# Kernel optimization log

Hardware: AMD Instinct MI355X
Metric: run time of the kernel (lower is better)

Reference implementation:

```python
import jax, jax.numpy as jnp
import numpy as np

N_NODES = 100000
N_EDGES = 1600000
NFEAT = 256
NHID = 128


def _l2_normalize(v, eps=1e-12):
    return v / (jnp.linalg.norm(v) + eps)


def setup_inputs() -> dict:
    key = jax.random.key(0)
    k1, k2, k3, k4 = jax.random.split(key, 4)
    x = jax.random.normal(k1, (N_NODES, NFEAT), dtype=jnp.float32)
    edge_index = jax.random.randint(k2, (2, N_EDGES), 0, N_NODES, dtype=jnp.int64)
    # GCNConv weight (glorot-ish scale), spectral-normalized at forward time
    W = jax.random.normal(k3, (NFEAT, NHID), dtype=jnp.float32) * 0.05
    bias = jnp.zeros((NHID,), dtype=jnp.float32)
    prelu_a = jnp.full((1,), 0.25, dtype=jnp.float32)  # nn.PReLU default slope
    u = _l2_normalize(jax.random.normal(k4, (NFEAT,), dtype=jnp.float32))
    return {"x": x, "edge_index": edge_index, "W": W, "bias": bias,
            "prelu_a": prelu_a, "u": u}


def reference(x, edge_index, W, bias, prelu_a, u):
    # --- spectral_norm: one power iteration (torch default n_power_iterations=1) ---
    v = _l2_normalize(W.T @ u)          # [NHID]
    u2 = _l2_normalize(W @ v)           # [NFEAT]
    sigma = u2 @ (W @ v)
    W_sn = W / sigma

    # --- GCNConv: linear transform, add self-loops, sym-normalize, scatter-add ---
    xw = x @ W_sn                       # [N, NHID]
    n = x.shape[0]
    loops = jnp.arange(n, dtype=edge_index.dtype)
    row = jnp.concatenate([edge_index[0], loops])  # sources
    col = jnp.concatenate([edge_index[1], loops])  # targets
    ones = jnp.ones(row.shape[0], dtype=x.dtype)
    deg = jax.ops.segment_sum(ones, col, num_segments=n)
    dinv = jnp.where(deg > 0, deg ** -0.5, 0.0)
    norm = dinv[row] * dinv[col]        # [E+N]
    msgs = norm[:, None] * xw[row]      # gather at sources
    out = jax.ops.segment_sum(msgs, col, num_segments=n) + bias

    # --- PReLU ---
    return jnp.where(out > 0, out, prelu_a * out)
```

## Files before the change

kernel.cpp:

```cpp
#include <hip/hip_runtime.h>

#define NFEAT 256
#define NHID  128

#define NBK   391
#define EPB   4096
#define NBLK  391

typedef __bf16 bf16x8 __attribute__((ext_vector_type(8)));
typedef __bf16 bf16x4 __attribute__((ext_vector_type(4)));
typedef float  f32x4  __attribute__((ext_vector_type(4)));

__global__ __launch_bounds__(256) void sigma_kernel(const float* __restrict__ W,
                                                    const float* __restrict__ u,
                                                    float* __restrict__ scal) {
    __shared__ float v[NHID];
    __shared__ float red[256];
    int tid = threadIdx.x;

    float t = 0.f;
    if (tid < NHID) {
        for (int i = 0; i < NFEAT; ++i) t += W[i * NHID + tid] * u[i];
    }
    red[tid] = (tid < NHID) ? t * t : 0.f;
    __syncthreads();
    for (int s = 128; s > 0; s >>= 1) {
        if (tid < s) red[tid] += red[tid + s];
        __syncthreads();
    }
    float nv = sqrtf(red[0]);
    float inv_nv = 1.f / (nv + 1e-12f);
    __syncthreads();
    if (tid < NHID) v[tid] = t * inv_nv;
    __syncthreads();

    float wv = 0.f;
    for (int j = 0; j < NHID; ++j) wv += W[tid * NHID + j] * v[j];
    red[tid] = wv * wv;
    __syncthreads();
    for (int s = 128; s > 0; s >>= 1) {
        if (tid < s) red[tid] += red[tid + s];
        __syncthreads();
    }
    if (tid == 0) {
        float n2  = red[0];
        float nwv = sqrtf(n2);
        float sigma = n2 / (nwv + 1e-12f);
        scal[0] = 1.f / sigma;
    }
}

__global__ __launch_bounds__(256) void wt_kernel(const float* __restrict__ W,
                                                 const float* __restrict__ scal,
                                                 __bf16* __restrict__ WT) {
    int idx = blockIdx.x * 256 + threadIdx.x;
    int c = idx >> 8;
    int r = idx & 255;
    WT[c * NFEAT + r] = (__bf16)(W[r * NHID + c] * scal[0]);
}

__global__ __launch_bounds__(256) void hist_kernel(const int* __restrict__ ecol,
                                                   int* __restrict__ blkhist, int E) {
    __shared__ int hist[NBK];
    int tid = threadIdx.x, b = blockIdx.x;
    for (int k = tid; k < NBK; k += 256) hist[k] = 0;
    __syncthreads();
    int e0 = b * EPB;
#pragma unroll
    for (int j = 0; j < 16; ++j) {
        int idx = e0 + j * 256 + tid;
        if (idx < E) atomicAdd(&hist[ecol[idx] >> 8], 1);
    }
    __syncthreads();
    for (int k = tid; k < NBK; k += 256) blkhist[k * NBLK + b] = hist[k];
}

__global__ __launch_bounds__(256) void scan_rows_kernel(int* __restrict__ blkhist,
                                                        int* __restrict__ btot) {
    int k = blockIdx.x * 4 + (threadIdx.x >> 6);
    int lane = threadIdx.x & 63;
    if (k >= NBK) return;
    int carry = 0;
    for (int c0 = 0; c0 < NBLK; c0 += 64) {
        int b = c0 + lane;
        int v = (b < NBLK) ? blkhist[k * NBLK + b] : 0;
        int orig = v;
#pragma unroll
        for (int d = 1; d < 64; d <<= 1) {
            int t = __shfl_up(v, (unsigned)d, 64);
            if (lane >= d) v += t;
        }
        if (b < NBLK) blkhist[k * NBLK + b] = carry + v - orig;
        carry += __shfl(v, 63, 64);
    }
    if (lane == 0) btot[k] = carry;
}

__global__ __launch_bounds__(512) void scan_buckets_kernel(const int* __restrict__ btot,
                                                           int* __restrict__ bbase) {
    __shared__ int s[512];
    int tid = threadIdx.x;
    int v = (tid < NBK) ? btot[tid] : 0;
    s[tid] = v;
    __syncthreads();
    int val = v;
    for (int off = 1; off < 512; off <<= 1) {
        int t = (tid >= off) ? s[tid - off] : 0;
        __syncthreads();
        val += t;
        s[tid] = val;
        __syncthreads();
    }
    if (tid <= NBK) bbase[tid] = val - v;
}

__global__ __launch_bounds__(512) void coarse_scatter_kernel(const int* __restrict__ erow,
                                                             const int* __restrict__ ecol,
                                                             const int* __restrict__ blkhist,
                                                             const int* __restrict__ bbase,
                                                             unsigned int* __restrict__ rbuf,
                                                             int E) {
    __shared__ unsigned int rec[EPB];
    __shared__ unsigned short bk[EPB];
    __shared__ int hist[NBK], sc[512], lbase[NBK], lfill[NBK], gb[NBK];
    int tid = threadIdx.x, b = blockIdx.x;
    for (int k = tid; k < NBK; k += 512) { hist[k] = 0; lfill[k] = 0; }
    __syncthreads();
    int e0 = b * EPB;
    unsigned int rv[8];
    int kv[8];
#pragma unroll
    for (int j = 0; j < 8; ++j) {
        int idx = e0 + j * 512 + tid;
        if (idx < E) {
            int c = ecol[idx];
            int s = erow[idx];
            int k = c >> 8;
            kv[j] = k;
            rv[j] = ((unsigned int)(c & 255) << 24) | (unsigned int)s;
            atomicAdd(&hist[k], 1);
        } else kv[j] = -1;
    }
    __syncthreads();
    int hv = (tid < NBK) ? hist[tid] : 0;
    sc[tid] = hv;
    __syncthreads();
    int val = hv;
    for (int off = 1; off < 512; off <<= 1) {
        int t = (tid >= off) ? sc[tid - off] : 0;
        __syncthreads();
        val += t;
        sc[tid] = val;
        __syncthreads();
    }
    if (tid < NBK) {
        lbase[tid] = val - hv;
        gb[tid] = bbase[tid] + blkhist[tid * NBLK + b];
    }
    __syncthreads();
#pragma unroll
    for (int j = 0; j < 8; ++j) {
        if (kv[j] >= 0) {
            int p = lbase[kv[j]] + atomicAdd(&lfill[kv[j]], 1);
            rec[p] = rv[j];
            bk[p] = (unsigned short)kv[j];
        }
    }
    __syncthreads();
    int nval = E - e0;
    if (nval > EPB) nval = EPB;
    for (int p = tid; p < nval; p += 512) {
        int k = bk[p];
        rbuf[gb[k] + (p - lbase[k])] = rec[p];
    }
}

__global__ __launch_bounds__(256) void fine_kernel(const unsigned int* __restrict__ rbuf,
                                                   const int* __restrict__ bbase,
                                                   int* __restrict__ base_g,
                                                   int* __restrict__ cnt_g,
                                                   float* __restrict__ dinv,
                                                   int* __restrict__ ebuf, int n) {
    __shared__ int cnt[256], lb[256], lf[256], sc[256];
    int tid = threadIdx.x, k = blockIdx.x;
    int seg0 = bbase[k], seg1 = bbase[k + 1];
    cnt[tid] = 0;
    lf[tid] = 0;
    __syncthreads();
    for (int j = seg0 + tid; j < seg1; j += 256)
        atomicAdd(&cnt[rbuf[j] >> 24], 1);
    __syncthreads();
    int cv = cnt[tid];
    sc[tid] = cv;
    __syncthreads();
    int val = cv;
    for (int off = 1; off < 256; off <<= 1) {
        int t = (tid >= off) ? sc[tid - off] : 0;
        __syncthreads();
        val += t;
        sc[tid] = val;
        __syncthreads();
    }
    lb[tid] = val - cv;
    __syncthreads();
    int node = k * 256 + tid;
    if (node < n) {
        base_g[node] = seg0 + lb[tid];
        cnt_g[node] = cv;
        dinv[node] = rsqrtf((float)cv + 1.f);
    }
    for (int j = seg0 + tid; j < seg1; j += 256) {
        unsigned int r = rbuf[j];
        int dl = r >> 24;
        int p = seg0 + lb[dl] + atomicAdd(&lf[dl], 1);
        ebuf[p] = (int)(r & 0xFFFFFFu);
    }
}

__global__ __launch_bounds__(256) void gemm_mfma_kernel(const float* __restrict__ x,
                                                        const __bf16* __restrict__ WT,
                                                        const float* __restrict__ dinv,
                                                        __bf16* __restrict__ xwb, int nn) {
    __shared__ __bf16 xs[2][64][64];

    int tid  = threadIdx.x;
    int lane = tid & 63;
    int w    = tid >> 6;
    int rfrag = lane & 15;
    int kg    = lane >> 4;
    int row0 = blockIdx.x * 64;

    int srow = tid >> 2;
    int sseg = tid & 3;
    int gsrow = row0 + srow;
    if (gsrow >= nn) gsrow = nn - 1;
    const float4* sx = (const float4*)(x + (size_t)gsrow * NFEAT) + sseg * 4;
    int sslot = sseg * 2;
    int sr7 = srow & 7;

    int crow0 = (w & 1) * 32 + rfrag;
    int col0 = (w >> 1) * 64;
    int r0 = row0 + crow0;
    int r1 = r0 + 16;
    const __bf16* wb = WT + (size_t)(col0 + rfrag) * NFEAT + kg * 8;
    int cr7 = crow0 & 7;

    f32x4 acc0[4] = {};
    f32x4 acc1[4] = {};

    {
        float4 f0 = sx[0], f1 = sx[1], f2 = sx[2], f3 = sx[3];
        bf16x8 h0, h1;
        h0[0] = (__bf16)f0.x; h0[1] = (__bf16)f0.y; h0[2] = (__bf16)f0.z; h0[3] = (__bf16)f0.w;
        h0[4] = (__bf16)f1.x; h0[5] = (__bf16)f1.y; h0[6] = (__bf16)f1.z; h0[7] = (__bf16)f1.w;
        h1[0] = (__bf16)f2.x; h1[1] = (__bf16)f2.y; h1[2] = (__bf16)f2.z; h1[3] = (__bf16)f2.w;
        h1[4] = (__bf16)f3.x; h1[5] = (__bf16)f3.y; h1[6] = (__bf16)f3.z; h1[7] = (__bf16)f3.w;
        *(bf16x8*)&xs[0][srow][(sslot ^ sr7) * 8]       = h0;
        *(bf16x8*)&xs[0][srow][((sslot + 1) ^ sr7) * 8] = h1;
    }
    __syncthreads();

#pragma unroll
    for (int c = 0; c < 4; ++c) {
        const int cur = c & 1;

        float4 f0, f1, f2, f3;
        if (c < 3) {
            const float4* p = sx + (c + 1) * 16;
            f0 = p[0]; f1 = p[1]; f2 = p[2]; f3 = p[3];
        }

#pragma unroll
        for (int ks = 0; ks < 2; ++ks) {
            int slog = ks * 4 + kg;
            bf16x8 af0 = *(const bf16x8*)&xs[cur][crow0][(slog ^ cr7) * 8];
            bf16x8 af1 = *(const bf16x8*)&xs[cur][crow0 + 16][(slog ^ cr7) * 8];
            int koff = c * 64 + ks * 32;
#pragma unroll
            for (int nt = 0; nt < 4; ++nt) {
                bf16x8 bf = *(const bf16x8*)(wb + (size_t)nt * 16 * NFEAT + koff);
                acc0[nt] = __builtin_amdgcn_mfma_f32_16x16x32_bf16(bf, af0, acc0[nt], 0, 0, 0);
                acc1[nt] = __builtin_amdgcn_mfma_f32_16x16x32_bf16(bf, af1, acc1[nt], 0, 0, 0);
            }
        }

        if (c < 3) {
            bf16x8 h0, h1;
            h0[0] = (__bf16)f0.x; h0[1] = (__bf16)f0.y; h0[2] = (__bf16)f0.z; h0[3] = (__bf16)f0.w;
            h0[4] = (__bf16)f1.x; h0[5] = (__bf16)f1.y; h0[6] = (__bf16)f1.z; h0[7] = (__bf16)f1.w;
            h1[0] = (__bf16)f2.x; h1[1] = (__bf16)f2.y; h1[2] = (__bf16)f2.z; h1[3] = (__bf16)f2.w;
            h1[4] = (__bf16)f3.x; h1[5] = (__bf16)f3.y; h1[6] = (__bf16)f3.z; h1[7] = (__bf16)f3.w;
            *(bf16x8*)&xs[cur ^ 1][srow][(sslot ^ sr7) * 8]       = h0;
            *(bf16x8*)&xs[cur ^ 1][srow][((sslot + 1) ^ sr7) * 8] = h1;
        }
        __syncthreads();
    }

    if (r0 < nn) {
        float d = dinv[r0];
        __bf16* orow = xwb + (size_t)r0 * NHID + col0 + kg * 4;
#pragma unroll
        for (int nt = 0; nt < 4; ++nt) {
            bf16x4 v;
            v[0] = (__bf16)(acc0[nt][0] * d);
            v[1] = (__bf16)(acc0[nt][1] * d);
            v[2] = (__bf16)(acc0[nt][2] * d);
            v[3] = (__bf16)(acc0[nt][3] * d);
            *(bf16x4*)&orow[nt * 16] = v;
        }
    }
    if (r1 < nn) {
        float d = dinv[r1];
        __bf16* orow = xwb + (size_t)r1 * NHID + col0 + kg * 4;
#pragma unroll
        for (int nt = 0; nt < 4; ++nt) {
            bf16x4 v;
            v[0] = (__bf16)(acc1[nt][0] * d);
            v[1] = (__bf16)(acc1[nt][1] * d);
            v[2] = (__bf16)(acc1[nt][2] * d);
            v[3] = (__bf16)(acc1[nt][3] * d);
            *(bf16x4*)&orow[nt * 16] = v;
        }
    }
}

__global__ __launch_bounds__(256) void gather_kernel(const uint4* __restrict__ xb4,
                                                     const int* __restrict__ base,
                                                     const int* __restrict__ cnt,
                                                     const int* __restrict__ ebuf,
                                                     const float* __restrict__ dinv,
                                                     const float* __restrict__ bias,
                                                     const float* __restrict__ pa,
                                                     float* __restrict__ out, int n) {
    int tid = threadIdx.x;
    int sub = tid & 15;
    int node = (blockIdx.x * 256 + tid) >> 4;
    if (node >= n) return;

    int b = base[node];
    int deg = cnt[node];

    uint4 s0 = xb4[(size_t)node * 16 + sub];
    float a0 = __uint_as_float(s0.x << 16);
    float a1 = __uint_as_float(s0.x & 0xffff0000u);
    float a2 = __uint_as_float(s0.y << 16);
    float a3 = __uint_as_float(s0.y & 0xffff0000u);
    float a4 = __uint_as_float(s0.z << 16);
    float a5 = __uint_as_float(s0.z & 0xffff0000u);
    float a6 = __uint_as_float(s0.w << 16);
    float a7 = __uint_as_float(s0.w & 0xffff0000u);

    int k = 0;
    for (; k + 4 <= deg; k += 4) {
        int r0 = ebuf[b + k + 0];
        int r1 = ebuf[b + k + 1];
        int r2 = ebuf[b + k + 2];
        int r3 = ebuf[b + k + 3];
        uint4 v0 = xb4[(size_t)r0 * 16 + sub];
        uint4 v1 = xb4[(size_t)r1 * 16 + sub];
        uint4 v2 = xb4[(size_t)r2 * 16 + sub];
        uint4 v3 = xb4[(size_t)r3 * 16 + sub];
        a0 += __uint_as_float(v0.x << 16) + __uint_as_float(v1.x << 16)
            + __uint_as_float(v2.x << 16) + __uint_as_float(v3.x << 16);
        a1 += __uint_as_float(v0.x & 0xffff0000u) + __uint_as_float(v1.x & 0xffff0000u)
            + __uint_as_float(v2.x & 0xffff0000u) + __uint_as_float(v3.x & 0xffff0000u);
        a2 += __uint_as_float(v0.y << 16) + __uint_as_float(v1.y << 16)
            + __uint_as_float(v2.y << 16) + __uint_as_float(v3.y << 16);
        a3 += __uint_as_float(v0.y & 0xffff0000u) + __uint_as_float(v1.y & 0xffff0000u)
            + __uint_as_float(v2.y & 0xffff0000u) + __uint_as_float(v3.y & 0xffff0000u);
        a4 += __uint_as_float(v0.z << 16) + __uint_as_float(v1.z << 16)
            + __uint_as_float(v2.z << 16) + __uint_as_float(v3.z << 16);
        a5 += __uint_as_float(v0.z & 0xffff0000u) + __uint_as_float(v1.z & 0xffff0000u)
            + __uint_as_float(v2.z & 0xffff0000u) + __uint_as_float(v3.z & 0xffff0000u);
        a6 += __uint_as_float(v0.w << 16) + __uint_as_float(v1.w << 16)
            + __uint_as_float(v2.w << 16) + __uint_as_float(v3.w << 16);
        a7 += __uint_as_float(v0.w & 0xffff0000u) + __uint_as_float(v1.w & 0xffff0000u)
            + __uint_as_float(v2.w & 0xffff0000u) + __uint_as_float(v3.w & 0xffff0000u);
    }
    for (; k < deg; ++k) {
        int r = ebuf[b + k];
        uint4 v = xb4[(size_t)r * 16 + sub];
        a0 += __uint_as_float(v.x << 16);
        a1 += __uint_as_float(v.x & 0xffff0000u);
        a2 += __uint_as_float(v.y << 16);
        a3 += __uint_as_float(v.y & 0xffff0000u);
        a4 += __uint_as_float(v.z << 16);
        a5 += __uint_as_float(v.z & 0xffff0000u);
        a6 += __uint_as_float(v.w << 16);
        a7 += __uint_as_float(v.w & 0xffff0000u);
    }

    float s = dinv[node];
    float alpha = pa[0];
    const float4* bb4 = (const float4*)bias;
    float4 b0 = bb4[sub * 2], b1 = bb4[sub * 2 + 1];
    float o0 = s * a0 + b0.x;
    float o1 = s * a1 + b0.y;
    float o2 = s * a2 + b0.z;
    float o3 = s * a3 + b0.w;
    float o4 = s * a4 + b1.x;
    float o5 = s * a5 + b1.y;
    float o6 = s * a6 + b1.z;
    float o7 = s * a7 + b1.w;
    o0 = o0 > 0.f ? o0 : alpha * o0;
    o1 = o1 > 0.f ? o1 : alpha * o1;
    o2 = o2 > 0.f ? o2 : alpha * o2;
    o3 = o3 > 0.f ? o3 : alpha * o3;
    o4 = o4 > 0.f ? o4 : alpha * o4;
    o5 = o5 > 0.f ? o5 : alpha * o5;
    o6 = o6 > 0.f ? o6 : alpha * o6;
    o7 = o7 > 0.f ? o7 : alpha * o7;
    float4* orow = (float4*)out + (size_t)node * 32 + sub * 2;
    orow[0] = make_float4(o0, o1, o2, o3);
    orow[1] = make_float4(o4, o5, o6, o7);
}

extern "C" void kernel_launch(void* const* d_in, const int* in_sizes, int n_in,
                              void* d_out, int out_size, void* d_ws, size_t ws_size,
                              hipStream_t stream) {
    const float* x    = (const float*)d_in[0];
    const int*   ei   = (const int*)d_in[1];
    const float* W    = (const float*)d_in[2];
    const float* bias = (const float*)d_in[3];
    const float* pa   = (const float*)d_in[4];
    const float* u    = (const float*)d_in[5];

    int n = in_sizes[0] / NFEAT;
    int e = in_sizes[1] / 2;
    const int* erow = ei;
    const int* ecol = ei + e;

    float* out = (float*)d_out;
    char* ws = (char*)d_ws;
    float*        scal   = (float*)(ws);
    int*          btot   = (int*)  (ws + 0x0001000);
    int*          bbase  = (int*)  (ws + 0x0002000);
    __bf16*       WT     = (__bf16*)(ws + 0x0010000);
    int*          base_g = (int*)  (ws + 0x0100000);
    int*          cnt_g  = (int*)  (ws + 0x0200000);
    float*        dinv   = (float*)(ws + 0x0300000);
    int*          blkhist= (int*)  (ws + 0x0400000);
    unsigned int* rbuf   = (unsigned int*)(ws + 0x0500000);
    int*          ebuf   = (int*)  (ws + 0x0C00000);
    __bf16*       xwb    = (__bf16*)(ws + 0x1300000);

    sigma_kernel<<<1, 256, 0, stream>>>(W, u, scal);
    wt_kernel<<<(NFEAT * NHID) / 256, 256, 0, stream>>>(W, scal, WT);

    hist_kernel<<<NBLK, 256, 0, stream>>>(ecol, blkhist, e);
    scan_rows_kernel<<<(NBK + 3) / 4, 256, 0, stream>>>(blkhist, btot);
    scan_buckets_kernel<<<1, 512, 0, stream>>>(btot, bbase);
    coarse_scatter_kernel<<<NBLK, 512, 0, stream>>>(erow, ecol, blkhist, bbase, rbuf, e);
    fine_kernel<<<NBK, 256, 0, stream>>>(rbuf, bbase, base_g, cnt_g, dinv, ebuf, n);

    gemm_mfma_kernel<<<(n + 63) / 64, 256, 0, stream>>>(x, WT, dinv, xwb, n);

    long long gunits = (long long)n * 16;
    gather_kernel<<<(int)((gunits + 255) / 256), 256, 0, stream>>>(
        (const uint4*)xwb, base_g, cnt_g, ebuf, dinv, bias, pa, out, n);
}
```

Baseline: 159.2 us.

## Stage x tiles into LDS via direct global_load_lds and convert to bf16 at read

Replaces the register-staged fp32-to-bf16 conversion and LDS store with direct global-to-LDS async loads of fp32 x rows, using an XOR swizzle in the source address. Conversion to bf16 now happens when fragments are read from LDS, and B fragments are preloaded per chunk. The aim is to free VGPRs and VALU work during staging and to overlap global loads with MFMA through explicit sched_barrier ordering. In exchange the LDS footprint doubles to fp32, which can lower occupancy, and every wave now repeats the conversion work.

```diff
diff --git a/kernel.cpp b/kernel.cpp
--- a/kernel.cpp
+++ b/kernel.cpp
@@ -221,7 +221,7 @@
                                                         const __bf16* __restrict__ WT,
                                                         const float* __restrict__ dinv,
                                                         __bf16* __restrict__ xwb, int nn) {
-    __shared__ __bf16 xs[2][64][64];
+    __shared__ float xs[2][64][64];
 
     int tid  = threadIdx.x;
     int lane = tid & 63;
@@ -230,16 +230,11 @@
     int kg    = lane >> 4;
     int row0 = blockIdx.x * 64;
 
-    int srow = tid >> 2;
-    int sseg = tid & 3;
-    int gsrow = row0 + srow;
-    if (gsrow >= nn) gsrow = nn - 1;
-    const float4* sx = (const float4*)(x + (size_t)gsrow * NFEAT) + sseg * 4;
-    int sslot = sseg * 2;
-    int sr7 = srow & 7;
+    int p16  = lane & 15;
+    int rsub = lane >> 4;
 
     int crow0 = (w & 1) * 32 + rfrag;
-    int col0 = (w >> 1) * 64;
+    int col0  = (w >> 1) * 64;
     int r0 = row0 + crow0;
     int r1 = r0 + 16;
     const __bf16* wb = WT + (size_t)(col0 + rfrag) * NFEAT + kg * 8;
@@ -248,53 +243,85 @@
     f32x4 acc0[4] = {};
     f32x4 acc1[4] = {};
 
-    {
-        float4 f0 = sx[0], f1 = sx[1], f2 = sx[2], f3 = sx[3];
-        bf16x8 h0, h1;
-        h0[0] = (__bf16)f0.x; h0[1] = (__bf16)f0.y; h0[2] = (__bf16)f0.z; h0[3] = (__bf16)f0.w;
-        h0[4] = (__bf16)f1.x; h0[5] = (__bf16)f1.y; h0[6] = (__bf16)f1.z; h0[7] = (__bf16)f1.w;
-        h1[0] = (__bf16)f2.x; h1[1] = (__bf16)f2.y; h1[2] = (__bf16)f2.z; h1[3] = (__bf16)f2.w;
-        h1[4] = (__bf16)f3.x; h1[5] = (__bf16)f3.y; h1[6] = (__bf16)f3.z; h1[7] = (__bf16)f3.w;
-        *(bf16x8*)&xs[0][srow][(sslot ^ sr7) * 8]       = h0;
-        *(bf16x8*)&xs[0][srow][((sslot + 1) ^ sr7) * 8] = h1;
-    }
-    __syncthreads();
-
-#pragma unroll
-    for (int c = 0; c < 4; ++c) {
-        const int cur = c & 1;
-
-        float4 f0, f1, f2, f3;
-        if (c < 3) {
-            const float4* p = sx + (c + 1) * 16;
-            f0 = p[0]; f1 = p[1]; f2 = p[2]; f3 = p[3];
-        }
-
+    auto STAGE = [&](int buf, int c) {
+#pragma unroll
+        for (int j = 0; j < 4; ++j) {
+            int rloc = w * 16 + j * 4 + rsub;
+            int grow = row0 + rloc;
+            if (grow >= nn) grow = nn - 1;
+            const float* src = x + (size_t)grow * NFEAT + c * 64 + ((p16 ^ (grow & 7)) << 2);
+            __builtin_amdgcn_global_load_lds(
+                (const __attribute__((address_space(1))) void*)src,
+                (__attribute__((address_space(3))) void*)&xs[buf][w * 16 + j * 4][0],
+                16, 0, 0);
+        }
+    };
+
+    bf16x8 Bf[2][4];
+    auto BLOAD = [&](int c) {
+#pragma unroll
+        for (int ks = 0; ks < 2; ++ks)
+#pragma unroll
+            for (int nt = 0; nt < 4; ++nt)
+                Bf[ks][nt] = *(const bf16x8*)(wb + (size_t)nt * 16 * NFEAT + c * 64 + ks * 32);
+    };
+
+    auto MFMA_CHUNK = [&](int buf) {
 #pragma unroll
         for (int ks = 0; ks < 2; ++ks) {
-            int slog = ks * 4 + kg;
-            bf16x8 af0 = *(const bf16x8*)&xs[cur][crow0][(slog ^ cr7) * 8];
-            bf16x8 af1 = *(const bf16x8*)&xs[cur][crow0 + 16][(slog ^ cr7) * 8];
-            int koff = c * 64 + ks * 32;
+            int sA = kg * 2 + ks * 8;
+            float4 a0lo = *(const float4*)&xs[buf][crow0][((sA) ^ cr7) * 4];
+            float4 a0hi = *(const float4*)&xs[buf][crow0][((sA + 1) ^ cr7) * 4];
+            float4 a1lo = *(const float4*)&xs[buf][crow0 + 16][((sA) ^ cr7) * 4];
+            float4 a1hi = *(const float4*)&xs[buf][crow0 + 16][((sA + 1) ^ cr7) * 4];
+            bf16x8 af0, af1;
+            af0[0] = (__bf16)a0lo.x; af0[1] = (__bf16)a0lo.y;
+            af0[2] = (__bf16)a0lo.z; af0[3] = (__bf16)a0lo.w;
+            af0[4] = (__bf16)a0hi.x; af0[5] = (__bf16)a0hi.y;
+            af0[6] = (__bf16)a0hi.z; af0[7] = (__bf16)a0hi.w;
+            af1[0] = (__bf16)a1lo.x; af1[1] = (__bf16)a1lo.y;
+            af1[2] = (__bf16)a1lo.z; af1[3] = (__bf16)a1lo.w;
+            af1[4] = (__bf16)a1hi.x; af1[5] = (__bf16)a1hi.y;
+            af1[6] = (__bf16)a1hi.z; af1[7] = (__bf16)a1hi.w;
 #pragma unroll
             for (int nt = 0; nt < 4; ++nt) {
-                bf16x8 bf = *(const bf16x8*)(wb + (size_t)nt * 16 * NFEAT + koff);
-                acc0[nt] = __builtin_amdgcn_mfma_f32_16x16x32_bf16(bf, af0, acc0[nt], 0, 0, 0);
-                acc1[nt] = __builtin_amdgcn_mfma_f32_16x16x32_bf16(bf, af1, acc1[nt], 0, 0, 0);
+                acc0[nt] = __builtin_amdgcn_mfma_f32_16x16x32_bf16(Bf[ks][nt], af0, acc0[nt], 0, 0, 0);
+                acc1[nt] = __builtin_amdgcn_mfma_f32_16x16x32_bf16(Bf[ks][nt], af1, acc1[nt], 0, 0, 0);
             }
         }
-
-        if (c < 3) {
-            bf16x8 h0, h1;
-            h0[0] = (__bf16)f0.x; h0[1] = (__bf16)f0.y; h0[2] = (__bf16)f0.z; h0[3] = (__bf16)f0.w;
-            h0[4] = (__bf16)f1.x; h0[5] = (__bf16)f1.y; h0[6] = (__bf16)f1.z; h0[7] = (__bf16)f1.w;
-            h1[0] = (__bf16)f2.x; h1[1] = (__bf16)f2.y; h1[2] = (__bf16)f2.z; h1[3] = (__bf16)f2.w;
-            h1[4] = (__bf16)f3.x; h1[5] = (__bf16)f3.y; h1[6] = (__bf16)f3.z; h1[7] = (__bf16)f3.w;
-            *(bf16x8*)&xs[cur ^ 1][srow][(sslot ^ sr7) * 8]       = h0;
-            *(bf16x8*)&xs[cur ^ 1][srow][((sslot + 1) ^ sr7) * 8] = h1;
-        }
-        __syncthreads();
-    }
+    };
+
+#define DRAIN_BAR() do { \
+        asm volatile("s_waitcnt vmcnt(0)" ::: "memory"); \
+        __builtin_amdgcn_s_barrier(); } while (0)
+
+    STAGE(0, 0);
+    DRAIN_BAR();
+
+    BLOAD(0);
+    __builtin_amdgcn_sched_barrier(0);
+    STAGE(1, 1);
+    __builtin_amdgcn_sched_barrier(0);
+    MFMA_CHUNK(0);
+    DRAIN_BAR();
+
+    BLOAD(1);
+    __builtin_amdgcn_sched_barrier(0);
+    STAGE(0, 2);
+    __builtin_amdgcn_sched_barrier(0);
+    MFMA_CHUNK(1);
+    DRAIN_BAR();
+
+    BLOAD(2);
+    __builtin_amdgcn_sched_barrier(0);
+    STAGE(1, 3);
+    __builtin_amdgcn_sched_barrier(0);
+    MFMA_CHUNK(0);
+    DRAIN_BAR();
+
+    BLOAD(3);
+    MFMA_CHUNK(1);
+#undef DRAIN_BAR
 
     if (r0 < nn) {
         float d = dinv[r0];
```

Result: no change. 157.3 us (-1.2%).
